# Performance work log

Hardware: AMD Instinct MI355X
Metric: run time of the kernel (lower is better)

## Reference

```python
import jax, jax.numpy as jnp
import numpy as np

IN_F = 256
OUT_F = 64
ALPHA = 0.2  # LeakyReLU negative slope
MASK_VAL = -9e15


def _glorot(key, shape):
    r = np.sqrt(6.0 / (shape[0] + shape[1]))
    return jax.random.uniform(key, shape, jnp.float32, -r, r)


def setup_inputs() -> dict:
    key = jax.random.key(0)
    k_h, k_adj, k_W, k_a = jax.random.split(key, 4)
    B, N = 4, 4096
    h = jax.random.normal(k_h, (B, N, IN_F), jnp.float32)
    adj = jax.random.randint(k_adj, (B, N, N), 0, 2, jnp.int32)
    W = _glorot(k_W, (IN_F, OUT_F))
    a = _glorot(k_a, (2 * OUT_F, 1))
    bias = jnp.zeros((OUT_F,), jnp.float32)
    return {"h": h, "adj": adj, "W": W, "a": a, "bias": bias}


def reference(h, adj, W, a, bias):
    # Wh: [B, N, F_out]
    Wh = jnp.matmul(h, W) + bias
    # additive attention: e_ij = leakyrelu(Wh_i . a1 + Wh_j . a2)
    Wh1 = jnp.matmul(Wh, a[:OUT_F, :])   # [B, N, 1]
    Wh2 = jnp.matmul(Wh, a[OUT_F:, :])   # [B, N, 1]
    e = Wh1 + jnp.swapaxes(Wh2, 2, 1)    # [B, N, N]
    e = jnp.where(e > 0, e, ALPHA * e)   # LeakyReLU
    e = jnp.where(adj > 0, e, MASK_VAL)
    attention = jax.nn.softmax(e, axis=2)
    h_prime = jnp.matmul(attention, Wh)  # [B, N, F_out]
    return jax.nn.elu(h_prime)           # concat=True -> ELU
```

## Files before the change

### kernel.cpp

```cpp
#include <hip/hip_runtime.h>
#include <hip/hip_bf16.h>
#include <cstdint>

#define IN_F 256
#define OUT_F 64
#define NB 4
#define NN 4096
#define ALPHA 0.2f

typedef __attribute__((ext_vector_type(4))) float f32x4;
typedef __attribute__((ext_vector_type(4))) int i32x4;
typedef __attribute__((ext_vector_type(8))) short bf16x8;

static __device__ __forceinline__ ushort f2bf(float x) {
  uint32_t u = __float_as_uint(x);
  uint32_t r = (u + 0x7fffu + ((u >> 16) & 1u)) >> 16;
  return (ushort)r;
}

static __device__ __forceinline__ void gl16(const void* g, void* l) {
  __builtin_amdgcn_global_load_lds(
      (const __attribute__((address_space(1))) void*)g,
      (__attribute__((address_space(3))) void*)l, 16, 0, 0);
}

__global__ __launch_bounds__(256) void k1_gemm(
    const float* __restrict__ h, const float* __restrict__ W,
    const float* __restrict__ a, const float* __restrict__ bias,
    ushort* __restrict__ WhT, float* __restrict__ Wh1, float* __restrict__ Wh2)
{
  __shared__ float hs[32][33];
  __shared__ float Ws[32][64];
  const int t  = threadIdx.x;
  const int tx = t & 15;
  const int ty = t >> 4;
  const int row0 = blockIdx.x * 32;

  float acc[2][4] = {};

  for (int k0 = 0; k0 < IN_F; k0 += 32) {
    {
      int r = t >> 3, c4 = t & 7;
      *(f32x4*)&hs[r][c4 * 4] =
          *(const f32x4*)(h + (size_t)(row0 + r) * IN_F + k0 + c4 * 4);
    }
    #pragma unroll
    for (int s = 0; s < 2; ++s) {
      int f4 = t + 256 * s;
      int kk = f4 >> 4, c4 = f4 & 15;
      *(f32x4*)&Ws[kk][c4 * 4] = *(const f32x4*)(W + (size_t)(k0 + kk) * OUT_F + c4 * 4);
    }
    __syncthreads();
    #pragma unroll 8
    for (int kk = 0; kk < 32; ++kk) {
      f32x4 bv = *(const f32x4*)&Ws[kk][tx * 4];
      float av0 = hs[ty * 2 + 0][kk];
      float av1 = hs[ty * 2 + 1][kk];
      #pragma unroll
      for (int j = 0; j < 4; ++j) {
        acc[0][j] += av0 * bv[j];
        acc[1][j] += av1 * bv[j];
      }
    }
    __syncthreads();
  }

  #pragma unroll
  for (int i = 0; i < 2; ++i) {
    int row = row0 + ty * 2 + i;
    float s1 = 0.f, s2 = 0.f;
    #pragma unroll
    for (int j = 0; j < 4; ++j) {
      float v = acc[i][j] + bias[tx * 4 + j];
      acc[i][j] = v;
      s1 += v * a[tx * 4 + j];
      s2 += v * a[64 + tx * 4 + j];
    }
    #pragma unroll
    for (int off = 1; off < 16; off <<= 1) {
      s1 += __shfl_xor(s1, off);
      s2 += __shfl_xor(s2, off);
    }
    if (tx == 0) { Wh1[row] = s1; Wh2[row] = s2; }
    int bb = row >> 12;
    int n  = row & 4095;
    #pragma unroll
    for (int j = 0; j < 4; ++j) {
      WhT[(((size_t)(bb * OUT_F + tx * 4 + j)) << 12) + n] = f2bf(acc[i][j]);
    }
  }
}

__global__ __launch_bounds__(256) void k1b_max(const float* __restrict__ Wh2,
                                               float* __restrict__ M2)
{
  const int b = blockIdx.x;
  float m = -3.0e38f;
  for (int i = threadIdx.x; i < NN; i += 256) m = fmaxf(m, Wh2[(b << 12) + i]);
  #pragma unroll
  for (int off = 1; off < 64; off <<= 1) m = fmaxf(m, __shfl_xor(m, off));
  __shared__ float sm[4];
  if ((threadIdx.x & 63) == 0) sm[threadIdx.x >> 6] = m;
  __syncthreads();
  if (threadIdx.x == 0) M2[b] = fmaxf(fmaxf(sm[0], sm[1]), fmaxf(sm[2], sm[3]));
}

#define BUFSZ 24576
#define WH2_OFF 73728
__global__ __launch_bounds__(512) void k2_attn(
    const int* __restrict__ adj, const ushort* __restrict__ WhT,
    const float* __restrict__ Wh1, const float* __restrict__ Wh2,
    const float* __restrict__ M2, float* __restrict__ out)
{
  extern __shared__ char smem[];
  const int t  = threadIdx.x;
  const int l  = t & 63;
  const int w  = t >> 6;
  const int rq = w >> 1;
  const int kq = w & 1;
  const int g  = l >> 4;
  const int lr = l & 15;
  const int b  = blockIdx.y;
  const int r0 = blockIdx.x << 6;

  const float LOG2E = 1.4426950408889634f;
  const int   rowl  = rq * 16 + lr;
  const float wh1 = Wh1[(b << 12) + r0 + rowl];
  float mr = wh1 + M2[b];
  mr = mr > 0.f ? mr : ALPHA * mr;
  const float nm2 = -mr * LOG2E;
  asm volatile("" :: "v"(nm2), "v"(wh1));

  const int*    adjb = adj + ((size_t)b << 24) + ((size_t)r0 << 12);
  const ushort* whb  = WhT + ((size_t)(b * OUT_F) << 12);
  const int rowA = t >> 4,           mlA = (t & 15) ^ (rowA & 7);
  const int rowB = (t + 512) >> 4,   mlB = (t & 15) ^ (rowB & 7);
  const int fW   = t >> 3,           mlW = (t & 7) ^ (fW & 7);
  const int*    srcA = adjb + (size_t)rowA * 4096 + mlA * 4;
  const int*    srcB = adjb + (size_t)rowB * 4096 + mlB * 4;
  const ushort* srcW = whb + ((size_t)fW << 12) + mlW * 8;
  const int ldsA = t << 4, ldsB = (t + 512) << 4, ldsW = 16384 + (t << 4);

  auto STAGE = [&](int s) {
    char* base = smem + (s % 3) * BUFSZ;
    gl16(srcA + s * 64, base + ldsA);
    gl16(srcB + s * 64, base + ldsB);
    gl16(srcW + s * 64, base + ldsW);
  };

  f32x4 a0 = {0.f,0.f,0.f,0.f}, a1 = {0.f,0.f,0.f,0.f};
  f32x4 a2 = {0.f,0.f,0.f,0.f}, a3 = {0.f,0.f,0.f,0.f};
  f32x4 as = {0.f,0.f,0.f,0.f};
  bf16x8 ones;
  #pragma unroll
  for (int i = 0; i < 8; ++i) ones[i] = (short)0x3F80;

  const int swzA = (rowl & 7) << 4;
  const int swzW = (lr & 7) << 4;
  const int offA0 = (kq * 128 + g * 32) ^ swzA;
  const int offA1 = (kq * 128 + g * 32 + 16) ^ swzA;
  const int offW  = (kq * 64 + g * 16) ^ swzW;

  auto COMPUTE = [&](int s) {
    const char* base = smem + (s % 3) * BUFSZ;
    i32x4 ad0 = *(const i32x4*)(base + rowl * 256 + offA0);
    i32x4 ad1 = *(const i32x4*)(base + rowl * 256 + offA1);
    const char* wb = base + 16384;
    bf16x8 b0 = *(const bf16x8*)(wb + (lr     ) * 128 + offW);
    bf16x8 b1 = *(const bf16x8*)(wb + (lr + 16) * 128 + offW);
    bf16x8 b2 = *(const bf16x8*)(wb + (lr + 32) * 128 + offW);
    bf16x8 b3 = *(const bf16x8*)(wb + (lr + 48) * 128 + offW);
    const char* w2b = smem + WH2_OFF + (s << 8) + kq * 128 + g * 32;
    f32x4 w20 = *(const f32x4*)(w2b);
    f32x4 w21 = *(const f32x4*)(w2b + 16);

    float p[8];
    #pragma unroll
    for (int i = 0; i < 8; ++i) {
      float w2 = (i < 4) ? w20[i] : w21[i - 4];
      int   am = (i < 4) ? ad0[i] : ad1[i - 4];
      float s_ = wh1 + w2;
      float lk = fmaf(ALPHA, fminf(s_, 0.f), fmaxf(s_, 0.f));
      float pe = exp2f(fmaf(lk, LOG2E, nm2));
      p[i] = (am > 0) ? pe : 0.0f;
    }
    union { bf16x8 v; uint32_t u[4]; } af;
    #pragma unroll
    for (int i = 0; i < 4; ++i)
      asm("v_cvt_pk_bf16_f32 %0, %1, %2" : "=v"(af.u[i]) : "v"(p[2*i]), "v"(p[2*i+1]));

    as = __builtin_amdgcn_mfma_f32_16x16x32_bf16(af.v, ones, as, 0, 0, 0);
    a0 = __builtin_amdgcn_mfma_f32_16x16x32_bf16(af.v, b0,   a0, 0, 0, 0);
    a1 = __builtin_amdgcn_mfma_f32_16x16x32_bf16(af.v, b1,   a1, 0, 0, 0);
    a2 = __builtin_amdgcn_mfma_f32_16x16x32_bf16(af.v, b2,   a2, 0, 0, 0);
    a3 = __builtin_amdgcn_mfma_f32_16x16x32_bf16(af.v, b3,   a3, 0, 0, 0);
  };

  {
    const float* w2src = Wh2 + (b << 12);
    gl16(w2src + (t << 2),         smem + WH2_OFF + (t << 4));
    gl16(w2src + ((t + 512) << 2), smem + WH2_OFF + ((t + 512) << 4));
  }
  STAGE(0);
  STAGE(1);

  for (int s = 0; s < 64; ++s) {
    if (s < 63) asm volatile("s_waitcnt vmcnt(3)" ::: "memory");
    else        asm volatile("s_waitcnt vmcnt(0)" ::: "memory");
    __builtin_amdgcn_s_barrier();
    asm volatile("" ::: "memory");
    COMPUTE(s);
    if (s < 62) STAGE(s + 2);
  }

  __syncthreads();
  float* sacc = (float*)smem;
  float* ssum = (float*)(smem + 34816);
  #pragma unroll
  for (int r = 0; r < 4; ++r) {
    int rr = rq * 16 + g * 4 + r;
    float* dst = sacc + (kq * 64 + rr) * 68;
    dst[ 0 + lr] = a0[r];
    dst[16 + lr] = a1[r];
    dst[32 + lr] = a2[r];
    dst[48 + lr] = a3[r];
    if (lr == 0) ssum[kq * 64 + rr] = as[r];
  }
  __syncthreads();

  const int row = t >> 3;
  const int c0  = (t & 7) << 3;
  const float* p0 = sacc + row * 68;
  const float* p1 = sacc + (64 + row) * 68;
  float d = ssum[row] + ssum[64 + row];
  float inv = 1.0f / d;
  f32x4 o0, o1;
  #pragma unroll
  for (int j = 0; j < 4; ++j) {
    float x = (p0[c0 + j] + p1[c0 + j]) * inv;
    o0[j] = x > 0.f ? x : expm1f(x);
    float y = (p0[c0 + 4 + j] + p1[c0 + 4 + j]) * inv;
    o1[j] = y > 0.f ? y : expm1f(y);
  }
  size_t ob = ((size_t)((b << 12) + r0 + row) << 6) + c0;
  *(f32x4*)(out + ob)     = o0;
  *(f32x4*)(out + ob + 4) = o1;
}

extern "C" void kernel_launch(void* const* d_in, const int* in_sizes, int n_in,
                              void* d_out, int out_size, void* d_ws, size_t ws_size,
                              hipStream_t stream) {
  const float* h    = (const float*)d_in[0];
  const int*   adj  = (const int*)d_in[1];
  const float* W    = (const float*)d_in[2];
  const float* a    = (const float*)d_in[3];
  const float* bias = (const float*)d_in[4];
  float* out = (float*)d_out;

  char* ws = (char*)d_ws;
  ushort* WhT = (ushort*)ws;
  float*  Wh1 = (float*)(ws + (size_t)NB * OUT_F * NN * 2);
  float*  Wh2 = Wh1 + NB * NN;
  float*  M2  = Wh2 + NB * NN;

  k1_gemm<<<dim3(NB * NN / 32), 256, 0, stream>>>(h, W, a, bias, WhT, Wh1, Wh2);
  k1b_max<<<dim3(NB), 256, 0, stream>>>(Wh2, M2);
  k2_attn<<<dim3(NN / 64, NB), 512, 90112, stream>>>(adj, WhT, Wh1, Wh2, M2, out);
}
```

Before: 78.16 us.

## Deepen adjacency prefetch pipeline to five stages and drop softmax max-shift kernel

Replaces the three-buffer LDS ring with a five-buffer ring that keeps four stages of adjacency/WhT loads in flight, with adjusted vmcnt waits, so more HBM latency is hidden behind compute. Removes the separate row-max reduction kernel and the max subtraction inside the exponent, computing exp of the raw LeakyReLU score. This saves a launch and a dependency, but risks overflow or precision loss when scores are large. LDS use rises to about 136KB, which needs the max dynamic shared memory attribute and limits occupancy to one block per CU.

```diff
diff --git a/kernel.cpp b/kernel.cpp
--- a/kernel.cpp
+++ b/kernel.cpp
@@ -91,26 +91,14 @@
   }
 }
 
-__global__ __launch_bounds__(256) void k1b_max(const float* __restrict__ Wh2,
-                                               float* __restrict__ M2)
-{
-  const int b = blockIdx.x;
-  float m = -3.0e38f;
-  for (int i = threadIdx.x; i < NN; i += 256) m = fmaxf(m, Wh2[(b << 12) + i]);
-  #pragma unroll
-  for (int off = 1; off < 64; off <<= 1) m = fmaxf(m, __shfl_xor(m, off));
-  __shared__ float sm[4];
-  if ((threadIdx.x & 63) == 0) sm[threadIdx.x >> 6] = m;
-  __syncthreads();
-  if (threadIdx.x == 0) M2[b] = fmaxf(fmaxf(sm[0], sm[1]), fmaxf(sm[2], sm[3]));
-}
-
 #define BUFSZ 24576
-#define WH2_OFF 73728
+#define NDEPTH 5
+#define WH2_OFF 122880
+#define LDS_TOTAL 139264
 __global__ __launch_bounds__(512) void k2_attn(
     const int* __restrict__ adj, const ushort* __restrict__ WhT,
     const float* __restrict__ Wh1, const float* __restrict__ Wh2,
-    const float* __restrict__ M2, float* __restrict__ out)
+    float* __restrict__ out)
 {
   extern __shared__ char smem[];
   const int t  = threadIdx.x;
@@ -126,10 +114,7 @@
   const float LOG2E = 1.4426950408889634f;
   const int   rowl  = rq * 16 + lr;
   const float wh1 = Wh1[(b << 12) + r0 + rowl];
-  float mr = wh1 + M2[b];
-  mr = mr > 0.f ? mr : ALPHA * mr;
-  const float nm2 = -mr * LOG2E;
-  asm volatile("" :: "v"(nm2), "v"(wh1));
+  asm volatile("" :: "v"(wh1));
 
   const int*    adjb = adj + ((size_t)b << 24) + ((size_t)r0 << 12);
   const ushort* whb  = WhT + ((size_t)(b * OUT_F) << 12);
@@ -142,7 +127,7 @@
   const int ldsA = t << 4, ldsB = (t + 512) << 4, ldsW = 16384 + (t << 4);
 
   auto STAGE = [&](int s) {
-    char* base = smem + (s % 3) * BUFSZ;
+    char* base = smem + (s % NDEPTH) * BUFSZ;
     gl16(srcA + s * 64, base + ldsA);
     gl16(srcB + s * 64, base + ldsB);
     gl16(srcW + s * 64, base + ldsW);
@@ -162,7 +147,7 @@
   const int offW  = (kq * 64 + g * 16) ^ swzW;
 
   auto COMPUTE = [&](int s) {
-    const char* base = smem + (s % 3) * BUFSZ;
+    const char* base = smem + (s % NDEPTH) * BUFSZ;
     i32x4 ad0 = *(const i32x4*)(base + rowl * 256 + offA0);
     i32x4 ad1 = *(const i32x4*)(base + rowl * 256 + offA1);
     const char* wb = base + 16384;
@@ -181,7 +166,7 @@
       int   am = (i < 4) ? ad0[i] : ad1[i - 4];
       float s_ = wh1 + w2;
       float lk = fmaf(ALPHA, fminf(s_, 0.f), fmaxf(s_, 0.f));
-      float pe = exp2f(fmaf(lk, LOG2E, nm2));
+      float pe = exp2f(lk * LOG2E);
       p[i] = (am > 0) ? pe : 0.0f;
     }
     union { bf16x8 v; uint32_t u[4]; } af;
@@ -203,14 +188,17 @@
   }
   STAGE(0);
   STAGE(1);
+  STAGE(2);
+  STAGE(3);
 
   for (int s = 0; s < 64; ++s) {
-    if (s < 63) asm volatile("s_waitcnt vmcnt(3)" ::: "memory");
-    else        asm volatile("s_waitcnt vmcnt(0)" ::: "memory");
+    if (s < 61)      asm volatile("s_waitcnt vmcnt(9)" ::: "memory");
+    else if (s == 61) asm volatile("s_waitcnt vmcnt(6)" ::: "memory");
+    else if (s == 62) asm volatile("s_waitcnt vmcnt(3)" ::: "memory");
+    else              asm volatile("s_waitcnt vmcnt(0)" ::: "memory");
     __builtin_amdgcn_s_barrier();
-    asm volatile("" ::: "memory");
     COMPUTE(s);
-    if (s < 62) STAGE(s + 2);
+    if (s < 60) STAGE(s + 4);
   }
 
   __syncthreads();
@@ -261,9 +249,10 @@
   ushort* WhT = (ushort*)ws;
   float*  Wh1 = (float*)(ws + (size_t)NB * OUT_F * NN * 2);
   float*  Wh2 = Wh1 + NB * NN;
-  float*  M2  = Wh2 + NB * NN;
+
+  (void)hipFuncSetAttribute((const void*)k2_attn,
+                            hipFuncAttributeMaxDynamicSharedMemorySize, LDS_TOTAL);
 
   k1_gemm<<<dim3(NB * NN / 32), 256, 0, stream>>>(h, W, a, bias, WhT, Wh1, Wh2);
-  k1b_max<<<dim3(NB), 256, 0, stream>>>(Wh2, M2);
-  k2_attn<<<dim3(NN / 64, NB), 512, 90112, stream>>>(adj, WhT, Wh1, Wh2, M2, out);
-}
+  k2_attn<<<dim3(NN / 64, NB), 512, LDS_TOTAL, stream>>>(adj, WhT, Wh1, Wh2, out);
+}
```

Result: faster. 74.94 us (-4.1%).
